# Kernel optimization log

Measured on AMD Instinct MI355X. Metric: run time of the kernel, lower is better.

The kernel has to match this reference:

```python
import jax, jax.numpy as jnp
import numpy as np
from jax import lax

SCALES = (1, 4, 16, 64)
EPS = 1e-5
B, S, D, H, R, FF = 4, 1024, 512, 8, 4, 2048
C = D // len(SCALES)  # channels per temporal scale


def _ln(x, g, b):
    mu = jnp.mean(x, -1, keepdims=True)
    var = jnp.mean(jnp.square(x - mu), -1, keepdims=True)
    return (x - mu) * lax.rsqrt(var + EPS) * g + b


def _interp_linear(y, L_out):
    # y: [B, C, L_in]; torch F.interpolate(mode='linear', align_corners=False)
    L_in = y.shape[-1]
    if L_in == L_out:
        return y
    pos = (jnp.arange(L_out, dtype=jnp.float32) + 0.5) * (L_in / L_out) - 0.5
    pos = jnp.clip(pos, 0.0, L_in - 1)
    lo = jnp.floor(pos).astype(jnp.int32)
    hi = jnp.minimum(lo + 1, L_in - 1)
    w = (pos - lo.astype(jnp.float32))
    return y[..., lo] * (1.0 - w) + y[..., hi] * w


def _conv1d(x, w, b, stride):
    # x: [B, Cin, L], w: [Cout, Cin, K]
    y = lax.conv_general_dilated(x, w, window_strides=(stride,), padding='VALID',
                                 dimension_numbers=('NCH', 'OIH', 'NCH'))
    return y + b[None, :, None]


def setup_inputs() -> dict:
    key = jax.random.key(0)
    ks = jax.random.split(key, 40)
    n = lambda k, shp, s=0.02: jax.random.normal(k, shp, jnp.float32) * s
    inp = {}
    inp['x'] = jax.random.normal(ks[0], (B, S, D), jnp.float32)
    inp['resource_mask'] = jax.random.randint(ks[1], (B, S), 0, R, jnp.int32)
    inp['attention_mask'] = jnp.ones((B, S), jnp.int32)
    inp['wq'] = n(ks[2], (D, D)); inp['bq'] = jnp.zeros((D,), jnp.float32)
    inp['wk'] = n(ks[3], (D, D)); inp['bk'] = jnp.zeros((D,), jnp.float32)
    inp['wv'] = n(ks[4], (D, D)); inp['bv'] = jnp.zeros((D,), jnp.float32)
    inp['wo'] = n(ks[5], (D, D)); inp['bo'] = jnp.zeros((D,), jnp.float32)
    inp['rbias'] = jax.random.normal(ks[6], (H, R, R), jnp.float32)
    for i, sc in enumerate(SCALES):
        inp[f'cw{i}'] = n(ks[7 + i], (C, D, sc))
        inp[f'cb{i}'] = jnp.zeros((C,), jnp.float32)
    inp['fw'] = n(ks[12], (D, D)); inp['fb'] = jnp.zeros((D,), jnp.float32)
    inp['ltg'] = jnp.ones((D,), jnp.float32); inp['ltb'] = jnp.zeros((D,), jnp.float32)
    inp['n1g'] = jnp.ones((D,), jnp.float32); inp['n1b'] = jnp.zeros((D,), jnp.float32)
    inp['n2g'] = jnp.ones((D,), jnp.float32); inp['n2b'] = jnp.zeros((D,), jnp.float32)
    inp['fw1'] = n(ks[13], (FF, D)); inp['fb1'] = jnp.zeros((FF,), jnp.float32)
    inp['fw2'] = n(ks[14], (D, FF)); inp['fb2'] = jnp.zeros((D,), jnp.float32)
    inp['n3g'] = jnp.ones((D,), jnp.float32); inp['n3b'] = jnp.zeros((D,), jnp.float32)
    return inp


def reference(x, resource_mask, attention_mask, wq, bq, wk, bk, wv, bv, wo, bo, rbias,
              cw0, cb0, cw1, cb1, cw2, cb2, cw3, cb3, fw, fb, ltg, ltb,
              n1g, n1b, n2g, n2b, fw1, fb1, fw2, fb2, n3g, n3b):
    b_, s_, d_ = x.shape
    dk = d_ // H
    # --- ResourceAwareAttention (dropout = identity in eval) ---
    q = (x @ wq.T + bq).reshape(b_, s_, H, dk).transpose(0, 2, 1, 3)
    k = (x @ wk.T + bk).reshape(b_, s_, H, dk).transpose(0, 2, 1, 3)
    v = (x @ wv.T + bv).reshape(b_, s_, H, dk).transpose(0, 2, 1, 3)
    scores = jnp.einsum('bhid,bhjd->bhij', q, k) / jnp.sqrt(jnp.float32(dk))
    # vectorized resource-bias gather: bias[b,h,i,j] = rbias[h, rm[b,i], rm[b,j]]
    idx_h = jnp.arange(H)[None, :, None, None]
    idx_i = resource_mask[:, None, :, None]
    idx_j = resource_mask[:, None, None, :]
    scores = scores + rbias[idx_h, idx_i, idx_j]
    scores = jnp.where(attention_mask[:, None, None, :] == 0, -1e9, scores)
    attn = jax.nn.softmax(scores, axis=-1)
    o = jnp.einsum('bhij,bhjd->bhid', attn, v).transpose(0, 2, 1, 3).reshape(b_, s_, d_)
    attn_out = o @ wo.T + bo
    x = _ln(x + attn_out, n1g, n1b)
    # --- MultiScaleTemporalEncoder ---
    xc = x.transpose(0, 2, 1)  # [B, D, S]
    convs = ((cw0, cb0), (cw1, cb1), (cw2, cb2), (cw3, cb3))
    outs = []
    for sc, (w, bb) in zip(SCALES, convs):
        y = _conv1d(xc, w, bb, sc)  # [B, C, S/sc]
        outs.append(_interp_linear(y, s_))
    ms = jnp.concatenate(outs, axis=1).transpose(0, 2, 1)  # [B, S, D]
    fused = ms @ fw.T + fb
    temporal = _ln(x + fused, ltg, ltb)
    x = _ln(x + temporal, n2g, n2b)
    # --- FFN ---
    ff = jax.nn.relu(x @ fw1.T + fb1) @ fw2.T + fb2
    return _ln(x + ff, n3g, n3b)
```

## Files before the change

### kernel.cpp

```cpp
#include <hip/hip_runtime.h>
#include <math.h>

constexpr int B_ = 4, S_ = 1024, D_ = 512, H_ = 8, FF_ = 2048;
constexpr int DK_ = 64;
constexpr int C_ = 128;
constexpr int QKVLD = 1536;

typedef __bf16 bf16x8 __attribute__((ext_vector_type(8)));
typedef __bf16 bf16x4 __attribute__((ext_vector_type(4)));
typedef short short4v __attribute__((ext_vector_type(4)));
typedef float floatx4 __attribute__((ext_vector_type(4)));

__device__ __forceinline__ void g2l16(const __bf16* g, __bf16* l) {
  __builtin_amdgcn_global_load_lds(
      (__attribute__((address_space(1))) void*)(unsigned long long)g,
      (__attribute__((address_space(3))) void*)(unsigned int)(unsigned long long)l,
      16, 0, 0);
}

__device__ __forceinline__ int xcd_swz(int lin, int nwg) {
  return (lin & 7) * (nwg >> 3) + (lin >> 3);
}

template <bool OUTBF16, bool RELU, bool WRITEVT>
__global__ __launch_bounds__(256, 2) void mgemm(
    const __bf16* __restrict__ A, const __bf16* __restrict__ W,
    const float* __restrict__ bias, void* __restrict__ Yv,
    int M, int N, int K, int ldY, __bf16* __restrict__ VT) {
  __shared__ __bf16 As[2][128 * 64];
  __shared__ __bf16 Bs[2][128 * 64];
  const int tid = threadIdx.x;
  const int wave = tid >> 6, lane = tid & 63;
  const int nwg = gridDim.x * gridDim.y;
  const int lin = blockIdx.y * gridDim.x + blockIdx.x;
  const int swz = xcd_swz(lin, nwg);
  const int bm = (swz / gridDim.x) * 128, bn = (swz % gridDim.x) * 128;

  const int rsub = lane >> 3;
  const int gch = ((lane & 7) ^ rsub) * 8;
  const __bf16* gA = A + (size_t)(bm + wave * 32 + rsub) * K + gch;
  const __bf16* gB = W + (size_t)(bn + wave * 32 + rsub) * K + gch;

  const int mrow = lane & 15, g4 = lane >> 4;
  const int rsw = mrow & 7;
  const int wm = (wave & 1) * 64, wn = (wave >> 1) * 64;

  floatx4 acc[4][4];
#pragma unroll
  for (int mi = 0; mi < 4; mi++)
#pragma unroll
    for (int ni = 0; ni < 4; ni++) acc[mi][ni] = (floatx4){0.f, 0.f, 0.f, 0.f};

  const int nk = K >> 6;
  auto stage = [&](int buf, int kt) {
    const __bf16* ga = gA + (size_t)kt * 64;
    const __bf16* gb = gB + (size_t)kt * 64;
    __bf16* la = &As[buf][wave * 32 * 64];
    __bf16* lb = &Bs[buf][wave * 32 * 64];
#pragma unroll
    for (int i = 0; i < 4; i++) {
      g2l16(ga + (size_t)(i * 8) * K, la + i * 8 * 64);
      g2l16(gb + (size_t)(i * 8) * K, lb + i * 8 * 64);
    }
  };

  stage(0, 0);
  int cur = 0;
  for (int kk = 0; kk < nk; kk++) {
    __syncthreads();
    if (kk + 1 < nk) stage(cur ^ 1, kk + 1);
    const __bf16* Ab = As[cur];
    const __bf16* Bb = Bs[cur];
#pragma unroll
    for (int c = 0; c < 2; c++) {
      const int pc = (((c * 4 + g4) ^ rsw)) * 8;
      bf16x8 af[4], bfr[4];
#pragma unroll
      for (int mi = 0; mi < 4; mi++)
        af[mi] = *(const bf16x8*)(Ab + (wm + mi * 16 + mrow) * 64 + pc);
#pragma unroll
      for (int ni = 0; ni < 4; ni++)
        bfr[ni] = *(const bf16x8*)(Bb + (wn + ni * 16 + mrow) * 64 + pc);
#pragma unroll
      for (int mi = 0; mi < 4; mi++)
#pragma unroll
        for (int ni = 0; ni < 4; ni++)
          acc[mi][ni] = __builtin_amdgcn_mfma_f32_16x16x32_bf16(af[mi], bfr[ni], acc[mi][ni], 0, 0, 0);
    }
    cur ^= 1;
  }

  const int cc = lane & 15;
  const int r0 = (lane >> 4) * 4;
  float bv[4];
#pragma unroll
  for (int ni = 0; ni < 4; ni++) bv[ni] = bias[bn + wn + ni * 16 + cc];
#pragma unroll
  for (int mi = 0; mi < 4; mi++) {
#pragma unroll
    for (int ni = 0; ni < 4; ni++) {
      const int col = bn + wn + ni * 16 + cc;
      if (WRITEVT && col >= 1024) {
        const int h = (col - 1024) >> 6, d = (col - 1024) & 63;
        const int rowb = bm + wm + mi * 16 + r0;
        const int b = rowb >> 10, s = rowb & 1023;
        union { __bf16 hh[4]; unsigned long long u; } w;
#pragma unroll
        for (int i = 0; i < 4; i++) w.hh[i] = (__bf16)(acc[mi][ni][i] + bv[ni]);
        *(unsigned long long*)(VT + (size_t)(b * 8 + h) * 65536 + (size_t)d * 1024 + s) = w.u;
      } else {
#pragma unroll
        for (int i = 0; i < 4; i++) {
          float v = acc[mi][ni][i] + bv[ni];
          if (RELU) v = fmaxf(v, 0.f);
          const size_t row = bm + wm + mi * 16 + r0 + i;
          if (OUTBF16)
            ((__bf16*)Yv)[row * ldY + col] = (__bf16)v;
          else
            ((float*)Yv)[row * ldY + col] = v;
        }
      }
    }
  }
}

template <bool OUTBF16, bool RELU>
__global__ __launch_bounds__(256, 2) void mgemm64(
    const __bf16* __restrict__ A, const __bf16* __restrict__ W,
    const float* __restrict__ bias, void* __restrict__ Yv,
    int M, int N, int K, int ldY) {
  __shared__ __bf16 As[2][64 * 64];
  __shared__ __bf16 Bs[2][64 * 64];
  const int tid = threadIdx.x;
  const int wave = tid >> 6, lane = tid & 63;
  const int nwg = gridDim.x * gridDim.y;
  const int lin = blockIdx.y * gridDim.x + blockIdx.x;
  const int swz = xcd_swz(lin, nwg);
  const int bm = (swz / gridDim.x) * 64, bn = (swz % gridDim.x) * 64;

  const int rsub = lane >> 3;
  const int gch = ((lane & 7) ^ rsub) * 8;
  const __bf16* gA = A + (size_t)(bm + wave * 16 + rsub) * K + gch;
  const __bf16* gB = W + (size_t)(bn + wave * 16 + rsub) * K + gch;

  const int mrow = lane & 15, g4 = lane >> 4;
  const int rsw = mrow & 7;
  const int wm = (wave & 1) * 32, wn = (wave >> 1) * 32;

  floatx4 acc[2][2];
#pragma unroll
  for (int mi = 0; mi < 2; mi++)
#pragma unroll
    for (int ni = 0; ni < 2; ni++) acc[mi][ni] = (floatx4){0.f, 0.f, 0.f, 0.f};

  const int nk = K >> 6;
  auto stage = [&](int buf, int kt) {
    const __bf16* ga = gA + (size_t)kt * 64;
    const __bf16* gb = gB + (size_t)kt * 64;
    __bf16* la = &As[buf][wave * 16 * 64];
    __bf16* lb = &Bs[buf][wave * 16 * 64];
#pragma unroll
    for (int i = 0; i < 2; i++) {
      g2l16(ga + (size_t)(i * 8) * K, la + i * 8 * 64);
      g2l16(gb + (size_t)(i * 8) * K, lb + i * 8 * 64);
    }
  };

  stage(0, 0);
  int cur = 0;
  for (int kk = 0; kk < nk; kk++) {
    __syncthreads();
    if (kk + 1 < nk) stage(cur ^ 1, kk + 1);
    const __bf16* Ab = As[cur];
    const __bf16* Bb = Bs[cur];
#pragma unroll
    for (int c = 0; c < 2; c++) {
      const int pc = (((c * 4 + g4) ^ rsw)) * 8;
      bf16x8 af[2], bfr[2];
#pragma unroll
      for (int mi = 0; mi < 2; mi++)
        af[mi] = *(const bf16x8*)(Ab + (wm + mi * 16 + mrow) * 64 + pc);
#pragma unroll
      for (int ni = 0; ni < 2; ni++)
        bfr[ni] = *(const bf16x8*)(Bb + (wn + ni * 16 + mrow) * 64 + pc);
#pragma unroll
      for (int mi = 0; mi < 2; mi++)
#pragma unroll
        for (int ni = 0; ni < 2; ni++)
          acc[mi][ni] = __builtin_amdgcn_mfma_f32_16x16x32_bf16(af[mi], bfr[ni], acc[mi][ni], 0, 0, 0);
    }
    cur ^= 1;
  }

  const int cc = lane & 15;
  const int r0 = (lane >> 4) * 4;
  float bv[2];
#pragma unroll
  for (int ni = 0; ni < 2; ni++) bv[ni] = bias[bn + wn + ni * 16 + cc];
#pragma unroll
  for (int mi = 0; mi < 2; mi++) {
#pragma unroll
    for (int ni = 0; ni < 2; ni++) {
      const int col = bn + wn + ni * 16 + cc;
#pragma unroll
      for (int i = 0; i < 4; i++) {
        float v = acc[mi][ni][i] + bv[ni];
        if (RELU) v = fmaxf(v, 0.f);
        const size_t row = bm + wm + mi * 16 + r0 + i;
        if (OUTBF16)
          ((__bf16*)Yv)[row * ldY + col] = (__bf16)v;
        else
          ((float*)Yv)[row * ldY + col] = v;
      }
    }
  }
}

__global__ __launch_bounds__(256, 2) void cgemm3(
    const __bf16* __restrict__ A, const __bf16* __restrict__ w4,
    const __bf16* __restrict__ w16, const __bf16* __restrict__ w64,
    const __bf16* __restrict__ w1, const float* __restrict__ cb0,
    float* __restrict__ y1, float* __restrict__ y2, float* __restrict__ y3,
    __bf16* __restrict__ msb) {
  int id = xcd_swz(blockIdx.x, 448);
  const __bf16* W;
  float* yseg = nullptr;
  int K, bm, k0, nk;
  bool direct = false;
  if (id < 128) {
    W = w4; yseg = y1; K = 2048; bm = (id & 15) * 64; k0 = (id >> 4) * 256; nk = 4;
  } else if (id < 256) {
    id -= 128;
    W = w16; yseg = y2; K = 8192; bm = (id & 3) * 64; k0 = (id >> 2) * 256; nk = 4;
  } else if (id < 384) {
    id -= 256;
    W = w64; yseg = y3; K = 32768; bm = 0; k0 = id * 256; nk = 4;
  } else {
    id -= 384;
    W = w1; K = 512; bm = id * 64; k0 = 0; nk = 8; direct = true;
  }

  __shared__ __bf16 As[2][64 * 64];
  __shared__ __bf16 Bs[2][128 * 64];
  const int tid = threadIdx.x;
  const int wave = tid >> 6, lane = tid & 63;

  const int rsub = lane >> 3;
  const int gch = ((lane & 7) ^ rsub) * 8;
  const __bf16* gA = A + (size_t)(bm + wave * 16 + rsub) * K + k0 + gch;
  const __bf16* gB = W + (size_t)(wave * 32 + rsub) * K + k0 + gch;

  const int mrow = lane & 15, g4 = lane >> 4;
  const int rsw = mrow & 7;

  floatx4 acc[8];
#pragma unroll
  for (int nj = 0; nj < 8; nj++) acc[nj] = (floatx4){0.f, 0.f, 0.f, 0.f};

  auto stage = [&](int buf, int kt) {
    const size_t ko = (size_t)kt * 64;
#pragma unroll
    for (int i = 0; i < 2; i++)
      g2l16(gA + ko + (size_t)(i * 8) * K, &As[buf][(wave * 16 + i * 8) * 64]);
#pragma unroll
    for (int i = 0; i < 4; i++)
      g2l16(gB + ko + (size_t)(i * 8) * K, &Bs[buf][(wave * 32 + i * 8) * 64]);
  };

  stage(0, 0);
  int cur = 0;
  for (int kk = 0; kk < nk; kk++) {
    __syncthreads();
    if (kk + 1 < nk) stage(cur ^ 1, kk + 1);
    const __bf16* Ab = As[cur];
    const __bf16* Bb = Bs[cur];
#pragma unroll
    for (int c = 0; c < 2; c++) {
      const int pc = (((c * 4 + g4) ^ rsw)) * 8;
      bf16x8 af = *(const bf16x8*)(Ab + (wave * 16 + mrow) * 64 + pc);
#pragma unroll
      for (int nj = 0; nj < 8; nj++) {
        bf16x8 bfv = *(const bf16x8*)(Bb + (nj * 16 + mrow) * 64 + pc);
        acc[nj] = __builtin_amdgcn_mfma_f32_16x16x32_bf16(af, bfv, acc[nj], 0, 0, 0);
      }
    }
    cur ^= 1;
  }

  const int cc = lane & 15;
  const int r0 = (lane >> 4) * 4;
  if (direct) {
#pragma unroll
    for (int nj = 0; nj < 8; nj++) {
      const float bb = cb0[nj * 16 + cc];
#pragma unroll
      for (int i = 0; i < 4; i++)
        msb[(size_t)(bm + wave * 16 + r0 + i) * 512 + nj * 16 + cc] =
            (__bf16)(acc[nj][i] + bb);
    }
  } else {
#pragma unroll
    for (int nj = 0; nj < 8; nj++)
#pragma unroll
      for (int i = 0; i < 4; i++)
        atomicAdd(&yseg[(size_t)(bm + wave * 16 + r0 + i) * 128 + nj * 16 + cc],
                  acc[nj][i]);
  }
}

__global__ __launch_bounds__(256) void prep(
    const float* __restrict__ cw1, const float* __restrict__ cw2,
    const float* __restrict__ cw3, __bf16* __restrict__ wt4,
    __bf16* __restrict__ wt16, __bf16* __restrict__ wt64,
    const float* __restrict__ s0, const float* __restrict__ s1,
    const float* __restrict__ s2, const float* __restrict__ s3,
    const float* __restrict__ s4, const float* __restrict__ s5,
    const float* __restrict__ s6, const float* __restrict__ s7,
    const float* __restrict__ s8,
    __bf16* __restrict__ d0, __bf16* __restrict__ d1, __bf16* __restrict__ d2,
    __bf16* __restrict__ d3, __bf16* __restrict__ d4, __bf16* __restrict__ d5,
    __bf16* __restrict__ d6, __bf16* __restrict__ d7, __bf16* __restrict__ d8,
    const float* __restrict__ bq, const float* __restrict__ bk,
    const float* __restrict__ bv, float* __restrict__ bqkv,
    const float* __restrict__ cb1, const float* __restrict__ cb2,
    const float* __restrict__ cb3, float* __restrict__ yall) {
  __shared__ float Ts[4608];
  const int tid = threadIdx.x;
  if (blockIdx.x < 1408) {
    int id = blockIdx.x;
    const float* cw;
    __bf16* wt;
    int lg, c, d0i, TD, L;
    if (id < 128) {
      cw = cw1; wt = wt4; lg = 2; c = id; d0i = 0; TD = 512; L = 2048;
    } else if (id < 384) {
      id -= 128;
      cw = cw2; wt = wt16; lg = 4; c = id >> 1; d0i = (id & 1) * 256; TD = 256; L = 4096;
    } else {
      id -= 384;
      cw = cw3; wt = wt64; lg = 6; c = id >> 3; d0i = (id & 7) * 64; TD = 64; L = 4096;
    }
    const int sc = 1 << lg;
    const int KD = 512 << lg;
    const float* src = cw + (size_t)c * KD + (size_t)d0i * sc;

    for (int f = tid * 4; f < L; f += 1024) {
      const float4 v = *(const float4*)(src + f);
      const float vv[4] = {v.x, v.y, v.z, v.w};
#pragma unroll
      for (int j = 0; j < 4; j++) {
        const int idx = f + j;
        const int dl = idx >> lg, k = idx & (sc - 1);
        Ts[dl * (sc + 1) + k] = vv[j];
      }
    }
    __syncthreads();

    for (int w = tid * 8; w < L; w += 2048) {
      const int kpos = w / TD;
      const int dl0 = w - kpos * TD;
      union { __bf16 hh[8]; bf16x8 v; } u;
#pragma unroll
      for (int j = 0; j < 8; j++)
        u.hh[j] = (__bf16)Ts[(dl0 + j) * (sc + 1) + kpos];
      *(bf16x8*)(wt + (size_t)c * KD + kpos * 512 + d0i + dl0) = u.v;
    }
    return;
  }

  const int qd = (blockIdx.x - 1408) * 256 + tid;
  if (qd < 384) {
    const int i = qd * 4;
    const float* s;
    int off;
    if (i < 512) { s = bq; off = 0; }
    else if (i < 1024) { s = bk; off = 512; }
    else { s = bv; off = 1024; }
    *(float4*)(bqkv + i) = *(const float4*)(s + i - off);
  }
  if (qd < 172032) {
    float bb;
    if (qd < 131072) bb = cb1[qd & 127];
    else if (qd < 163840) bb = cb2[qd & 127];
    else bb = cb3[qd & 127];
    yall[qd] = bb;
  }
  if (qd >= 1392640) return;
  const float* src;
  __bf16* dst;
  int base;
  if (qd < 524288) { src = s0; dst = d0; base = 0; }
  else if (qd < 589824) { src = s1; dst = d1; base = 524288; }
  else if (qd < 655360) { src = s2; dst = d2; base = 589824; }
  else if (qd < 720896) { src = s3; dst = d3; base = 655360; }
  else if (qd < 786432) { src = s4; dst = d4; base = 720896; }
  else if (qd < 851968) { src = s5; dst = d5; base = 786432; }
  else if (qd < 868352) { src = s6; dst = d6; base = 851968; }
  else if (qd < 1130496) { src = s7; dst = d7; base = 868352; }
  else { src = s8; dst = d8; base = 1130496; }
  const int local = qd - base;
  float4 v = *(const float4*)(src + (size_t)local * 4);
  union { __bf16 h[4]; unsigned long long u; } t;
  t.h[0] = (__bf16)v.x; t.h[1] = (__bf16)v.y;
  t.h[2] = (__bf16)v.z; t.h[3] = (__bf16)v.w;
  *(unsigned long long*)(dst + (size_t)local * 4) = t.u;
}

__global__ __launch_bounds__(256) void fattn(
    const __bf16* __restrict__ QKV, const __bf16* __restrict__ VT,
    const float* __restrict__ rbias, const int* __restrict__ rm,
    const int* __restrict__ amask, __bf16* __restrict__ O) {
  __shared__ __bf16 Ks[2][64 * 64];
  __shared__ __bf16 Vs[2][64 * 64];
  __shared__ float T[4 * 1032];

  const int tid = threadIdx.x, wave = tid >> 6, lane = tid & 63;
  const int nwg = gridDim.x * gridDim.y;
  const int lin = blockIdx.y * gridDim.x + blockIdx.x;
  const int swz = xcd_swz(lin, nwg);
  const int qb = swz % gridDim.x;
  const int bh = swz / gridDim.x;
  const int b = bh >> 3, h = bh & 7;
  const int q0 = qb * 64;
  const int cc = lane & 15, quad = lane >> 4;

  for (int j = tid; j < 1024; j += 256) {
    const int rv = rm[b * S_ + j];
    const float mk = amask[b * S_ + j] ? 1.f : 0.f;
#pragma unroll
    for (int ri = 0; ri < 4; ri++)
      T[ri * 1032 + j] = __expf(rbias[h * 16 + ri * 4 + rv]) * mk;
  }

  const int qrow = q0 + wave * 16;
  const int rmi = rm[b * S_ + qrow + cc];
  const float* Trow = T + rmi * 1032;

  const __bf16* Qr = QKV + (size_t)(b * S_ + qrow + cc) * QKVLD + h * 64;
  const bf16x8 qb0 = *(const bf16x8*)(Qr + quad * 8);
  const bf16x8 qb1 = *(const bf16x8*)(Qr + 32 + quad * 8);

  floatx4 of[4];
#pragma unroll
  for (int dc = 0; dc < 4; dc++) of[dc] = (floatx4){0.f, 0.f, 0.f, 0.f};
  float mold = -1e30f, l = 0.f;

  const int rsub = lane >> 3;
  const int sgch = ((lane & 7) ^ rsub) * 8;
  const __bf16* Kg = QKV + (size_t)(b * S_ + wave * 16 + rsub) * QKVLD + 512 + h * 64 + sgch;
  const __bf16* Vg = VT + (size_t)bh * 65536 + (size_t)(wave * 16 + rsub) * 1024 + sgch;

  auto stage = [&](int buf, int jt) {
    const int j0 = jt * 64;
#pragma unroll
    for (int i = 0; i < 2; i++) {
      g2l16(Kg + (size_t)(j0 + i * 8) * QKVLD, &Ks[buf][(wave * 16 + i * 8) * 64]);
      g2l16(Vg + j0 + (size_t)(i * 8) * 1024, &Vs[buf][(wave * 16 + i * 8) * 64]);
    }
  };

  stage(0, 0);
  int cur = 0;
  const int rk = cc & 7;

  for (int jt = 0; jt < 16; jt++) {
    const int j0 = jt * 64;
    __syncthreads();
    if (jt + 1 < 16) stage(cur ^ 1, jt + 1);
    const __bf16* Kb = Ks[cur];
    const __bf16* Vb = Vs[cur];

    floatx4 st[4];
    __builtin_amdgcn_s_setprio(1);
#pragma unroll
    for (int js = 0; js < 4; js++) {
      const bf16x8 ka0 = *(const bf16x8*)(Kb + (js * 16 + cc) * 64 + ((quad ^ rk) * 8));
      const bf16x8 ka1 = *(const bf16x8*)(Kb + (js * 16 + cc) * 64 + (((quad + 4) ^ rk) * 8));
      floatx4 s = (floatx4){0.f, 0.f, 0.f, 0.f};
      s = __builtin_amdgcn_mfma_f32_16x16x32_bf16(ka0, qb0, s, 0, 0, 0);
      s = __builtin_amdgcn_mfma_f32_16x16x32_bf16(ka1, qb1, s, 0, 0, 0);
      st[js] = s;
    }
    __builtin_amdgcn_s_setprio(0);

    float mxr = st[0][0];
#pragma unroll
    for (int js = 0; js < 4; js++)
#pragma unroll
      for (int i = 0; i < 4; i++) mxr = fmaxf(mxr, st[js][i]);
    mxr = fmaxf(mxr, __shfl_xor(mxr, 16));
    mxr = fmaxf(mxr, __shfl_xor(mxr, 32));
    const float mnew = fmaxf(mold, mxr * 0.125f);
    const float alpha = __expf(mold - mnew);
    mold = mnew;

    float rsum = 0.f;
    short4v pk[4];
#pragma unroll
    for (int js = 0; js < 4; js++) {
      const floatx4 Tv = *(const floatx4*)(Trow + j0 + js * 16 + quad * 4);
      union { __bf16 hh[4]; short4v s4; } u;
#pragma unroll
      for (int i = 0; i < 4; i++) {
        const float p = __expf(fmaf(st[js][i], 0.125f, -mnew)) * Tv[i];
        rsum += p;
        u.hh[i] = (__bf16)p;
      }
      pk[js] = u.s4;
    }
    rsum += __shfl_xor(rsum, 16);
    rsum += __shfl_xor(rsum, 32);
    l = l * alpha + rsum;

#pragma unroll
    for (int dc = 0; dc < 4; dc++)
#pragma unroll
      for (int i = 0; i < 4; i++) of[dc][i] *= alpha;

    __builtin_amdgcn_s_setprio(1);
#pragma unroll
    for (int dc = 0; dc < 4; dc++) {
#pragma unroll
      for (int js = 0; js < 4; js++) {
        union { bf16x4 v; short4v s4; } va;
        va.v = *(const bf16x4*)(Vb + (dc * 16 + cc) * 64 +
                                (((js * 2 + (quad >> 1)) ^ rk) * 8) + (quad & 1) * 4);
        of[dc] = __builtin_amdgcn_mfma_f32_16x16x16bf16_1k(va.s4, pk[js], of[dc], 0, 0, 0);
      }
    }
    __builtin_amdgcn_s_setprio(0);
    cur ^= 1;
  }

  const float invl = 1.f / l;
  __bf16* po = O + (size_t)(b * S_ + qrow + cc) * D_ + h * 64;
#pragma unroll
  for (int dc = 0; dc < 4; dc++) {
    union { __bf16 hh[4]; unsigned long long u; } w;
#pragma unroll
    for (int i = 0; i < 4; i++) w.hh[i] = (__bf16)(of[dc][i] * invl);
    *(unsigned long long*)(po + dc * 16 + quad * 4) = w.u;
  }
}

__global__ __launch_bounds__(256) void add_ln_kernel(
    const float* __restrict__ xa, const float* __restrict__ xb,
    const float* __restrict__ g, const float* __restrict__ be,
    float* __restrict__ out, __bf16* __restrict__ outb) {
  const int row = (blockIdx.x * 256 + threadIdx.x) >> 6;
  const int lane = threadIdx.x & 63;
  const floatx4* pa = (const floatx4*)(xa + (size_t)row * D_);
  const floatx4* pb = (const floatx4*)(xb + (size_t)row * D_);
  floatx4 v[2];
  float sum = 0.f;
#pragma unroll
  for (int i = 0; i < 2; i++) {
    const int dd = lane + 64 * i;
    v[i] = pa[dd] + pb[dd];
    sum += v[i][0] + v[i][1] + v[i][2] + v[i][3];
  }
#pragma unroll
  for (int off = 32; off; off >>= 1) sum += __shfl_xor(sum, off);
  const float mu = sum * (1.f / D_);
  float vs = 0.f;
#pragma unroll
  for (int i = 0; i < 2; i++)
#pragma unroll
    for (int j = 0; j < 4; j++) { float t = v[i][j] - mu; vs += t * t; }
#pragma unroll
  for (int off = 32; off; off >>= 1) vs += __shfl_xor(vs, off);
  const float inv = rsqrtf(vs * (1.f / D_) + 1e-5f);
  floatx4* po = (floatx4*)(out + (size_t)row * D_);
#pragma unroll
  for (int i = 0; i < 2; i++) {
    const int dd = lane + 64 * i;
    const floatx4 g4 = ((const floatx4*)g)[dd];
    const floatx4 b4 = ((const floatx4*)be)[dd];
    const floatx4 o = (v[i] - mu) * inv * g4 + b4;
    po[dd] = o;
    if (outb) {
      union { __bf16 hh[4]; unsigned long long u; } w;
#pragma unroll
      for (int j = 0; j < 4; j++) w.hh[j] = (__bf16)o[j];
      *(unsigned long long*)(outb + (size_t)row * D_ + dd * 4) = w.u;
    }
  }
}

__global__ __launch_bounds__(256) void ln_chain_kernel(
    const float* __restrict__ x1, const float* __restrict__ fused,
    const float* __restrict__ ltg, const float* __restrict__ ltb,
    const float* __restrict__ n2g, const float* __restrict__ n2b,
    float* __restrict__ out, __bf16* __restrict__ outb) {
  const int row = (blockIdx.x * 256 + threadIdx.x) >> 6;
  const int lane = threadIdx.x & 63;
  const floatx4* p1 = (const floatx4*)(x1 + (size_t)row * D_);
  const floatx4* pf = (const floatx4*)(fused + (size_t)row * D_);
  floatx4 xv[2], u[2];
  float sum = 0.f;
#pragma unroll
  for (int i = 0; i < 2; i++) {
    const int dd = lane + 64 * i;
    xv[i] = p1[dd];
    u[i] = xv[i] + pf[dd];
    sum += u[i][0] + u[i][1] + u[i][2] + u[i][3];
  }
#pragma unroll
  for (int off = 32; off; off >>= 1) sum += __shfl_xor(sum, off);
  float mu = sum * (1.f / D_);
  float vs = 0.f;
#pragma unroll
  for (int i = 0; i < 2; i++)
#pragma unroll
    for (int j = 0; j < 4; j++) { float t = u[i][j] - mu; vs += t * t; }
#pragma unroll
  for (int off = 32; off; off >>= 1) vs += __shfl_xor(vs, off);
  float inv = rsqrtf(vs * (1.f / D_) + 1e-5f);
  float sum2 = 0.f;
#pragma unroll
  for (int i = 0; i < 2; i++) {
    const int dd = lane + 64 * i;
    const floatx4 g4 = ((const floatx4*)ltg)[dd];
    const floatx4 b4 = ((const floatx4*)ltb)[dd];
    u[i] = xv[i] + ((u[i] - mu) * inv * g4 + b4);
    sum2 += u[i][0] + u[i][1] + u[i][2] + u[i][3];
  }
#pragma unroll
  for (int off = 32; off; off >>= 1) sum2 += __shfl_xor(sum2, off);
  float mu2 = sum2 * (1.f / D_);
  float vs2 = 0.f;
#pragma unroll
  for (int i = 0; i < 2; i++)
#pragma unroll
    for (int j = 0; j < 4; j++) { float t = u[i][j] - mu2; vs2 += t * t; }
#pragma unroll
  for (int off = 32; off; off >>= 1) vs2 += __shfl_xor(vs2, off);
  float inv2 = rsqrtf(vs2 * (1.f / D_) + 1e-5f);
  floatx4* po = (floatx4*)(out + (size_t)row * D_);
#pragma unroll
  for (int i = 0; i < 2; i++) {
    const int dd = lane + 64 * i;
    const floatx4 g4 = ((const floatx4*)n2g)[dd];
    const floatx4 b4 = ((const floatx4*)n2b)[dd];
    const floatx4 o = (u[i] - mu2) * inv2 * g4 + b4;
    po[dd] = o;
    union { __bf16 hh[4]; unsigned long long u8; } w;
#pragma unroll
    for (int j = 0; j < 4; j++) w.hh[j] = (__bf16)o[j];
    *(unsigned long long*)(outb + (size_t)row * D_ + dd * 4) = w.u8;
  }
}

__global__ void interp_kernel(const float* __restrict__ y1, const float* __restrict__ y2,
                              const float* __restrict__ y3, __bf16* __restrict__ ms) {
  int idx = blockIdx.x * 256 + threadIdx.x;
  if (idx >= B_ * S_ * 3 * C_ / 4) return;
  const int c3_4 = idx % 96;
  const int rest = idx / 96;
  const int s = rest & 1023, b = rest >> 10;
  const int i = c3_4 >> 5;
  const int c = (c3_4 & 31) * 4;
  const int Lin = (i == 0) ? 256 : (i == 1) ? 64 : 16;
  const float* y = (i == 0) ? y1 : (i == 1) ? y2 : y3;
  float pos = (s + 0.5f) * ((float)Lin / S_) - 0.5f;
  pos = fminf(fmaxf(pos, 0.f), (float)(Lin - 1));
  const int lo = (int)floorf(pos);
  const int hi = min(lo + 1, Lin - 1);
  const float w = pos - (float)lo;
  const float* ybase = y + ((size_t)(b * Lin + lo)) * 128 + c;
  const floatx4 vlo = *(const floatx4*)ybase;
  const floatx4 vhi = *(const floatx4*)(ybase + (size_t)(hi - lo) * 128);
  const floatx4 o = vlo * (1.f - w) + vhi * w;
  union { __bf16 hh[4]; unsigned long long u; } t;
#pragma unroll
  for (int j = 0; j < 4; j++) t.hh[j] = (__bf16)o[j];
  *(unsigned long long*)(ms + ((size_t)b * S_ + s) * D_ + C_ + i * 128 + c) = t.u;
}

extern "C" void kernel_launch(void* const* d_in, const int* in_sizes, int n_in,
                              void* d_out, int out_size, void* d_ws, size_t ws_size,
                              hipStream_t stream) {
  const float* x   = (const float*)d_in[0];
  const int* rm    = (const int*)d_in[1];
  const int* am    = (const int*)d_in[2];
  const float* wq  = (const float*)d_in[3];
  const float* bq  = (const float*)d_in[4];
  const float* wk  = (const float*)d_in[5];
  const float* bk  = (const float*)d_in[6];
  const float* wv  = (const float*)d_in[7];
  const float* bv  = (const float*)d_in[8];
  const float* wo  = (const float*)d_in[9];
  const float* bo  = (const float*)d_in[10];
  const float* rbias = (const float*)d_in[11];
  const float* cw0 = (const float*)d_in[12];
  const float* cb0 = (const float*)d_in[13];
  const float* cw1 = (const float*)d_in[14];
  const float* cb1 = (const float*)d_in[15];
  const float* cw2 = (const float*)d_in[16];
  const float* cb2 = (const float*)d_in[17];
  const float* cw3 = (const float*)d_in[18];
  const float* cb3 = (const float*)d_in[19];
  const float* fw  = (const float*)d_in[20];
  const float* fb  = (const float*)d_in[21];
  const float* ltg = (const float*)d_in[22];
  const float* ltb = (const float*)d_in[23];
  const float* n1g = (const float*)d_in[24];
  const float* n1b = (const float*)d_in[25];
  const float* n2g = (const float*)d_in[26];
  const float* n2b = (const float*)d_in[27];
  const float* fw1 = (const float*)d_in[28];
  const float* fb1 = (const float*)d_in[29];
  const float* fw2 = (const float*)d_in[30];
  const float* fb2 = (const float*)d_in[31];
  const float* n3g = (const float*)d_in[32];
  const float* n3b = (const float*)d_in[33];

  float* ws = (float*)d_ws;
  __bf16* wqkvb = (__bf16*)(ws + 0);
  __bf16* wob   = (__bf16*)(ws + 393216);
  __bf16* fwb   = (__bf16*)(ws + 524288);
  __bf16* cw0b  = (__bf16*)(ws + 655360);
  __bf16* fw1b  = (__bf16*)(ws + 688128);
  __bf16* fw2b  = (__bf16*)(ws + 1212416);
  __bf16* xb    = (__bf16*)(ws + 1835008);
  __bf16* qkv   = (__bf16*)(ws + 2883584);
  __bf16* attnb = (__bf16*)(ws + 6029312);
  float*  x1    = ws + 7077888;
  __bf16* x1b   = (__bf16*)(ws + 9175040);
  float*  scr   = ws + 10223616;
  float*  x2    = ws + 12320768;
  __bf16* x2b   = (__bf16*)(ws + 14417920);
  __bf16* msb   = (__bf16*)(ws + 15466496);
  float*  y1    = ws + 16515072;
  float*  y2    = ws + 16646144;
  float*  y3    = ws + 16678912;
  float*  bqkv  = ws + 16687104;
  __bf16* wt4b  = (__bf16*)(ws + 16689152);
  __bf16* wt16b = (__bf16*)(ws + 16820224);
  __bf16* wt64b = (__bf16*)(ws + 17344512);
  __bf16* VT    = (__bf16*)(ws + 10223616);
  __bf16* ffh   = (__bf16*)(ws + 2883584);

  dim3 blk(256);

  prep<<<6848, blk, 0, stream>>>(
      cw1, cw2, cw3, wt4b, wt16b, wt64b,
      x, wq, wk, wv, wo, fw, cw0, fw1, fw2,
      xb, wqkvb, wqkvb + 262144, wqkvb + 524288, wob, fwb, cw0b, fw1b, fw2b,
      bq, bk, bv, bqkv, cb1, cb2, cb3, y1);

  mgemm<true, false, true><<<dim3(12, 32), blk, 0, stream>>>(
      xb, wqkvb, bqkv, qkv, 4096, 1536, 512, QKVLD, VT);

  fattn<<<dim3(16, 32), blk, 0, stream>>>(qkv, VT, rbias, rm, am, attnb);

  mgemm64<false, false><<<dim3(8, 64), blk, 0, stream>>>(
      attnb, wob, bo, scr, 4096, 512, 512, 512);
  add_ln_kernel<<<1024, blk, 0, stream>>>(x, scr, n1g, n1b, x1, x1b);

  cgemm3<<<448, blk, 0, stream>>>(x1b, wt4b, wt16b, wt64b, cw0b, cb0, y1, y2, y3, msb);
  interp_kernel<<<1536, blk, 0, stream>>>(y1, y2, y3, msb);

  mgemm64<false, false><<<dim3(8, 64), blk, 0, stream>>>(
      msb, fwb, fb, scr, 4096, 512, 512, 512);
  ln_chain_kernel<<<1024, blk, 0, stream>>>(x1, scr, ltg, ltb, n2g, n2b, x2, x2b);

  mgemm<true, true, false><<<dim3(16, 32), blk, 0, stream>>>(
      x2b, fw1b, fb1, ffh, 4096, 2048, 512, 2048, nullptr);
  mgemm64<false, false><<<dim3(8, 64), blk, 0, stream>>>(
      ffh, fw2b, fb2, scr, 4096, 512, 2048, 512);
  add_ln_kernel<<<1024, blk, 0, stream>>>(x2, scr, n3g, n3b, (float*)d_out, nullptr);
}
```

Before: 271.3 us.

## Split-K the N=512 GEMMs in two and fold partial sums into LayerNorm

The three 512-wide output GEMMs now split K into two halves across twice as many workgroups (1024 instead of 512). Each half writes raw fp32 partial sums to its own buffer, and the following add+LayerNorm kernels add both partials plus the bias. Occupancy hint raised to 4 blocks per CU. The aim is to fill the GPU better on these small-N GEMMs. The cost is an extra fp32 partial buffer that must be written and re-read, and reused workspace regions (ffh area, x1) serve as scratch.

```diff
diff --git a/kernel.cpp b/kernel.cpp
--- a/kernel.cpp
+++ b/kernel.cpp
@@ -124,11 +124,10 @@
   }
 }
 
-template <bool OUTBF16, bool RELU>
-__global__ __launch_bounds__(256, 2) void mgemm64(
+__global__ __launch_bounds__(256, 4) void mgemm64s(
     const __bf16* __restrict__ A, const __bf16* __restrict__ W,
-    const float* __restrict__ bias, void* __restrict__ Yv,
-    int M, int N, int K, int ldY) {
+    float* __restrict__ Y0, float* __restrict__ Y1,
+    int Kstride, int Khalf) {
   __shared__ __bf16 As[2][64 * 64];
   __shared__ __bf16 Bs[2][64 * 64];
   const int tid = threadIdx.x;
@@ -136,12 +135,17 @@
   const int nwg = gridDim.x * gridDim.y;
   const int lin = blockIdx.y * gridDim.x + blockIdx.x;
   const int swz = xcd_swz(lin, nwg);
-  const int bm = (swz / gridDim.x) * 64, bn = (swz % gridDim.x) * 64;
+  const int bn = (swz & 7) * 64;
+  const int rest = swz >> 3;
+  const int ks = rest & 1;
+  const int bm = (rest >> 1) * 64;
+  const int k0 = ks * Khalf;
+  float* __restrict__ Y = ks ? Y1 : Y0;
 
   const int rsub = lane >> 3;
   const int gch = ((lane & 7) ^ rsub) * 8;
-  const __bf16* gA = A + (size_t)(bm + wave * 16 + rsub) * K + gch;
-  const __bf16* gB = W + (size_t)(bn + wave * 16 + rsub) * K + gch;
+  const __bf16* gA = A + (size_t)(bm + wave * 16 + rsub) * Kstride + k0 + gch;
+  const __bf16* gB = W + (size_t)(bn + wave * 16 + rsub) * Kstride + k0 + gch;
 
   const int mrow = lane & 15, g4 = lane >> 4;
   const int rsw = mrow & 7;
@@ -153,7 +157,7 @@
 #pragma unroll
     for (int ni = 0; ni < 2; ni++) acc[mi][ni] = (floatx4){0.f, 0.f, 0.f, 0.f};
 
-  const int nk = K >> 6;
+  const int nk = Khalf >> 6;
   auto stage = [&](int buf, int kt) {
     const __bf16* ga = gA + (size_t)kt * 64;
     const __bf16* gb = gB + (size_t)kt * 64;
@@ -161,8 +165,8 @@
     __bf16* lb = &Bs[buf][wave * 16 * 64];
 #pragma unroll
     for (int i = 0; i < 2; i++) {
-      g2l16(ga + (size_t)(i * 8) * K, la + i * 8 * 64);
-      g2l16(gb + (size_t)(i * 8) * K, lb + i * 8 * 64);
+      g2l16(ga + (size_t)(i * 8) * Kstride, la + i * 8 * 64);
+      g2l16(gb + (size_t)(i * 8) * Kstride, lb + i * 8 * 64);
     }
   };
 
@@ -194,9 +198,6 @@
 
   const int cc = lane & 15;
   const int r0 = (lane >> 4) * 4;
-  float bv[2];
-#pragma unroll
-  for (int ni = 0; ni < 2; ni++) bv[ni] = bias[bn + wn + ni * 16 + cc];
 #pragma unroll
   for (int mi = 0; mi < 2; mi++) {
 #pragma unroll
@@ -204,13 +205,8 @@
       const int col = bn + wn + ni * 16 + cc;
 #pragma unroll
       for (int i = 0; i < 4; i++) {
-        float v = acc[mi][ni][i] + bv[ni];
-        if (RELU) v = fmaxf(v, 0.f);
         const size_t row = bm + wm + mi * 16 + r0 + i;
-        if (OUTBF16)
-          ((__bf16*)Yv)[row * ldY + col] = (__bf16)v;
-        else
-          ((float*)Yv)[row * ldY + col] = v;
+        Y[row * 512 + col] = acc[mi][ni][i];
       }
     }
   }
@@ -544,19 +540,21 @@
 }
 
 __global__ __launch_bounds__(256) void add_ln_kernel(
-    const float* __restrict__ xa, const float* __restrict__ xb,
+    const float* __restrict__ xa, const float* __restrict__ h0,
+    const float* __restrict__ h1, const float* __restrict__ bias,
     const float* __restrict__ g, const float* __restrict__ be,
     float* __restrict__ out, __bf16* __restrict__ outb) {
   const int row = (blockIdx.x * 256 + threadIdx.x) >> 6;
   const int lane = threadIdx.x & 63;
   const floatx4* pa = (const floatx4*)(xa + (size_t)row * D_);
-  const floatx4* pb = (const floatx4*)(xb + (size_t)row * D_);
+  const floatx4* p0 = (const floatx4*)(h0 + (size_t)row * D_);
+  const floatx4* p1 = (const floatx4*)(h1 + (size_t)row * D_);
   floatx4 v[2];
   float sum = 0.f;
 #pragma unroll
   for (int i = 0; i < 2; i++) {
     const int dd = lane + 64 * i;
-    v[i] = pa[dd] + pb[dd];
+    v[i] = pa[dd] + p0[dd] + p1[dd] + ((const floatx4*)bias)[dd];
     sum += v[i][0] + v[i][1] + v[i][2] + v[i][3];
   }
 #pragma unroll
@@ -588,21 +586,23 @@
 }
 
 __global__ __launch_bounds__(256) void ln_chain_kernel(
-    const float* __restrict__ x1, const float* __restrict__ fused,
+    const float* __restrict__ x1, const float* __restrict__ h0,
+    const float* __restrict__ h1, const float* __restrict__ bias,
     const float* __restrict__ ltg, const float* __restrict__ ltb,
     const float* __restrict__ n2g, const float* __restrict__ n2b,
     float* __restrict__ out, __bf16* __restrict__ outb) {
   const int row = (blockIdx.x * 256 + threadIdx.x) >> 6;
   const int lane = threadIdx.x & 63;
   const floatx4* p1 = (const floatx4*)(x1 + (size_t)row * D_);
-  const floatx4* pf = (const floatx4*)(fused + (size_t)row * D_);
+  const floatx4* pf0 = (const floatx4*)(h0 + (size_t)row * D_);
+  const floatx4* pf1 = (const floatx4*)(h1 + (size_t)row * D_);
   floatx4 xv[2], u[2];
   float sum = 0.f;
 #pragma unroll
   for (int i = 0; i < 2; i++) {
     const int dd = lane + 64 * i;
     xv[i] = p1[dd];
-    u[i] = xv[i] + pf[dd];
+    u[i] = xv[i] + pf0[dd] + pf1[dd] + ((const floatx4*)bias)[dd];
     sum += u[i][0] + u[i][1] + u[i][2] + u[i][3];
   }
 #pragma unroll
@@ -740,6 +740,7 @@
   __bf16* wt64b = (__bf16*)(ws + 17344512);
   __bf16* VT    = (__bf16*)(ws + 10223616);
   __bf16* ffh   = (__bf16*)(ws + 2883584);
+  float*  h1a   = ws + 2883584;
 
   dim3 blk(256);
 
@@ -754,20 +755,17 @@
 
   fattn<<<dim3(16, 32), blk, 0, stream>>>(qkv, VT, rbias, rm, am, attnb);
 
-  mgemm64<false, false><<<dim3(8, 64), blk, 0, stream>>>(
-      attnb, wob, bo, scr, 4096, 512, 512, 512);
-  add_ln_kernel<<<1024, blk, 0, stream>>>(x, scr, n1g, n1b, x1, x1b);
+  mgemm64s<<<dim3(8, 128), blk, 0, stream>>>(attnb, wob, scr, h1a, 512, 256);
+  add_ln_kernel<<<1024, blk, 0, stream>>>(x, scr, h1a, bo, n1g, n1b, x1, x1b);
 
   cgemm3<<<448, blk, 0, stream>>>(x1b, wt4b, wt16b, wt64b, cw0b, cb0, y1, y2, y3, msb);
   interp_kernel<<<1536, blk, 0, stream>>>(y1, y2, y3, msb);
 
-  mgemm64<false, false><<<dim3(8, 64), blk, 0, stream>>>(
-      msb, fwb, fb, scr, 4096, 512, 512, 512);
-  ln_chain_kernel<<<1024, blk, 0, stream>>>(x1, scr, ltg, ltb, n2g, n2b, x2, x2b);
+  mgemm64s<<<dim3(8, 128), blk, 0, stream>>>(msb, fwb, scr, h1a, 512, 256);
+  ln_chain_kernel<<<1024, blk, 0, stream>>>(x1, scr, h1a, fb, ltg, ltb, n2g, n2b, x2, x2b);
 
   mgemm<true, true, false><<<dim3(16, 32), blk, 0, stream>>>(
       x2b, fw1b, fb1, ffh, 4096, 2048, 512, 2048, nullptr);
-  mgemm64<false, false><<<dim3(8, 64), blk, 0, stream>>>(
-      ffh, fw2b, fb2, scr, 4096, 512, 2048, 512);
-  add_ln_kernel<<<1024, blk, 0, stream>>>(x2, scr, n3g, n3b, (float*)d_out, nullptr);
-}
+  mgemm64s<<<dim3(8, 128), blk, 0, stream>>>(ffh, fw2b, scr, x1, 2048, 1024);
+  add_ln_kernel<<<1024, blk, 0, stream>>>(x2, scr, x1, fb2, n3g, n3b, (float*)d_out, nullptr);
+}
```

New measurement: 268.9 us. About the same (-0.9%).
